# Kernel optimization log

Measured on AMD Instinct MI355X. Metric: run time of the kernel, lower is better.

## Reference

```python
import jax, jax.numpy as jnp
import numpy as np

N, E, T, B = 10000, 80000, 240000, 32
HF, EMB = 256, 64
EDGE_BINS, ANG_BINS = 80, 40
N_CONV = 12  # 4 alignn layers x 2 EGGC + 4 gcn EGGC


def layernorm(x, scale, bias):
    m = x.mean(-1, keepdims=True)
    v = ((x - m) ** 2).mean(-1, keepdims=True)
    return (x - m) / jnp.sqrt(v + 1e-5) * scale + bias


def mlp_layer(x, W, b, ln):
    # Linear -> LayerNorm -> SiLU
    return jax.nn.silu(layernorm(x @ W + b, ln[0], ln[1]))


def rbf(x, vmin, vmax, bins):
    centers = jnp.linspace(vmin, vmax, bins)
    gamma = 0.5 / ((vmax - vmin) / bins) ** 2
    return jnp.exp(-gamma * (x[..., None] - centers) ** 2)


def eggc(W, b, ln_s, ln_b, src, dst, h, e, n_nodes):
    """Edge-gated graph conv. W:[5,F,F] b:[5,F] order: src_gate,dst_gate,edge_gate,src_update,dst_update.
    ln_s/ln_b:[2,F] order: edges, nodes."""
    e_src = h @ W[0] + b[0]
    e_dst = h @ W[1] + b[1]
    sigma = jax.nn.sigmoid(e_src[src] + e_dst[dst] + e @ W[2] + b[2])  # [n_edges, F]
    e_out = layernorm(sigma * e, ln_s[0], ln_b[0])
    Bh = h @ W[4] + b[4]  # dst_update
    sum_sh = jax.ops.segment_sum(Bh[src] * sigma, dst, num_segments=n_nodes)
    sum_s = jax.ops.segment_sum(sigma, dst, num_segments=n_nodes)
    h_out = h @ W[3] + b[3] + sum_sh / (sum_s + 1e-8)  # src_update + gated mean
    return layernorm(h_out, ln_s[1], ln_b[1]), e_out


def setup_inputs() -> dict:
    key = jax.random.key(0)
    ks = jax.random.split(key, 24)
    rn = lambda k, shp: (jax.random.normal(k, shp, dtype=jnp.float32) * 0.05)
    ln_init = lambda f: jnp.stack([jnp.ones((f,), jnp.float32), jnp.zeros((f,), jnp.float32)])
    inp = {
        'atom_features': jax.random.normal(ks[0], (N, 92), dtype=jnp.float32),
        'bondlength': jax.random.uniform(ks[1], (E,), dtype=jnp.float32) * 8.0,
        'angle_h': jax.random.uniform(ks[2], (T,), dtype=jnp.float32) * 2.0 - 1.0,
        'src': jax.random.randint(ks[3], (E,), 0, N, dtype=jnp.int32),
        'dst': jax.random.randint(ks[4], (E,), 0, N, dtype=jnp.int32),
        'lg_src': jax.random.randint(ks[5], (T,), 0, E, dtype=jnp.int32),
        'lg_dst': jax.random.randint(ks[6], (T,), 0, E, dtype=jnp.int32),
        'graph_ids': jnp.sort(jax.random.randint(ks[7], (N,), 0, B)).astype(jnp.int32),
        'atom_W': rn(ks[8], (92, HF)), 'atom_b': jnp.zeros((HF,), jnp.float32), 'atom_ln': ln_init(HF),
        'edge_W1': rn(ks[9], (EDGE_BINS, EMB)), 'edge_b1': jnp.zeros((EMB,), jnp.float32), 'edge_ln1': ln_init(EMB),
        'edge_W2': rn(ks[10], (EMB, HF)), 'edge_b2': jnp.zeros((HF,), jnp.float32), 'edge_ln2': ln_init(HF),
        'ang_W1': rn(ks[11], (ANG_BINS, EMB)), 'ang_b1': jnp.zeros((EMB,), jnp.float32), 'ang_ln1': ln_init(EMB),
        'ang_W2': rn(ks[12], (EMB, HF)), 'ang_b2': jnp.zeros((HF,), jnp.float32), 'ang_ln2': ln_init(HF),
        'conv_W': rn(ks[13], (N_CONV, 5, HF, HF)),
        'conv_b': jnp.zeros((N_CONV, 5, HF), jnp.float32),
        'conv_ln_s': jnp.ones((N_CONV, 2, HF), jnp.float32),
        'conv_ln_b': jnp.zeros((N_CONV, 2, HF), jnp.float32),
    }
    return inp


def reference(atom_features, bondlength, angle_h, src, dst, lg_src, lg_dst, graph_ids,
              atom_W, atom_b, atom_ln, edge_W1, edge_b1, edge_ln1, edge_W2, edge_b2, edge_ln2,
              ang_W1, ang_b1, ang_ln1, ang_W2, ang_b2, ang_ln2,
              conv_W, conv_b, conv_ln_s, conv_ln_b):
    n_nodes = atom_features.shape[0]
    n_edges = bondlength.shape[0]
    # embeddings
    z = mlp_layer(mlp_layer(rbf(angle_h, -1.0, 1.0, ANG_BINS), ang_W1, ang_b1, ang_ln1), ang_W2, ang_b2, ang_ln2)
    x = mlp_layer(atom_features, atom_W, atom_b, atom_ln)
    y = mlp_layer(mlp_layer(rbf(bondlength, 0.0, 8.0, EDGE_BINS), edge_W1, edge_b1, edge_ln1), edge_W2, edge_b2, edge_ln2)
    # 4 ALIGNN layers: edge_update on line graph, then node_update on graph
    for i in range(4):
        j = 2 * i
        y, z = eggc(conv_W[j], conv_b[j], conv_ln_s[j], conv_ln_b[j], lg_src, lg_dst, y, z, n_edges)
        j = 2 * i + 1
        x, y = eggc(conv_W[j], conv_b[j], conv_ln_s[j], conv_ln_b[j], src, dst, x, y, n_nodes)
    # 4 GCN layers
    for i in range(4):
        j = 8 + i
        x, y = eggc(conv_W[j], conv_b[j], conv_ln_s[j], conv_ln_b[j], src, dst, x, y, n_nodes)
    # AvgPooling readout per graph
    sums = jax.ops.segment_sum(x, graph_ids, num_segments=B)
    counts = jax.ops.segment_sum(jnp.ones((n_nodes,), x.dtype), graph_ids, num_segments=B)
    return sums / jnp.maximum(counts, 1.0)[:, None]
```

## Files before the change

kernel.cpp:

```cpp
#include <hip/hip_runtime.h>
#include <hip/hip_bf16.h>

typedef unsigned short u16;
typedef unsigned int u32;
typedef __attribute__((ext_vector_type(8))) short short8;
typedef __attribute__((ext_vector_type(4))) float f32x4;

__device__ __forceinline__ float bf2f(u16 u) { return __uint_as_float(((u32)u) << 16); }
__device__ __forceinline__ u16 f2bf(float f) {
  u32 x = __float_as_uint(f);
  return (u16)((x + 0x7FFFu + ((x >> 16) & 1u)) >> 16);
}
__device__ __forceinline__ void up4(uint2 r, float* o) {
  o[0] = bf2f((u16)(r.x & 0xFFFF)); o[1] = bf2f((u16)(r.x >> 16));
  o[2] = bf2f((u16)(r.y & 0xFFFF)); o[3] = bf2f((u16)(r.y >> 16));
}
__device__ __forceinline__ uint2 pk4(const float* o) {
  uint2 r;
  r.x = (u32)f2bf(o[0]) | ((u32)f2bf(o[1]) << 16);
  r.y = (u32)f2bf(o[2]) | ((u32)f2bf(o[3]) << 16);
  return r;
}
__device__ __forceinline__ void up8(uint4 r, float* o) {
  o[0] = bf2f((u16)(r.x & 0xFFFF)); o[1] = bf2f((u16)(r.x >> 16));
  o[2] = bf2f((u16)(r.y & 0xFFFF)); o[3] = bf2f((u16)(r.y >> 16));
  o[4] = bf2f((u16)(r.z & 0xFFFF)); o[5] = bf2f((u16)(r.z >> 16));
  o[6] = bf2f((u16)(r.w & 0xFFFF)); o[7] = bf2f((u16)(r.w >> 16));
}
__device__ __forceinline__ uint4 pk8(const float* o) {
  uint4 r;
  r.x = (u32)f2bf(o[0]) | ((u32)f2bf(o[1]) << 16);
  r.y = (u32)f2bf(o[2]) | ((u32)f2bf(o[3]) << 16);
  r.z = (u32)f2bf(o[4]) | ((u32)f2bf(o[5]) << 16);
  r.w = (u32)f2bf(o[6]) | ((u32)f2bf(o[7]) << 16);
  return r;
}
__device__ __forceinline__ float wsum64(float v) {
#pragma unroll
  for (int o = 32; o > 0; o >>= 1) v += __shfl_xor(v, o, 64);
  return v;
}
__device__ __forceinline__ float wsum16(float v) {
#pragma unroll
  for (int o = 8; o > 0; o >>= 1) v += __shfl_xor(v, o, 64);
  return v;
}
__device__ __forceinline__ float sigm(float x) { return 1.0f / (1.0f + __expf(-x)); }

__global__ __launch_bounds__(256) void fill_kernel(float* __restrict__ out, int n, float v) {
  int i = blockIdx.x * 256 + threadIdx.x;
  if (i < n) out[i] = v;
}

__global__ __launch_bounds__(256) void wtrans(const float* __restrict__ in,
                                              u16* __restrict__ out, int R, int Ccols) {
  __shared__ float t[64][65];
  const float* ip = in + (size_t)blockIdx.z * R * Ccols;
  u16* op = out + (size_t)blockIdx.z * R * Ccols;
  int kb = blockIdx.x * 64, nb = blockIdx.y * 64;
  int lr = threadIdx.x >> 4, lc = (threadIdx.x & 15) * 4;
#pragma unroll
  for (int p = 0; p < 4; ++p) {
    int k = lr + p * 16;
    float4 v = *(const float4*)(ip + (size_t)(kb + k) * Ccols + nb + lc);
    t[k][lc + 0] = v.x; t[k][lc + 1] = v.y; t[k][lc + 2] = v.z; t[k][lc + 3] = v.w;
  }
  __syncthreads();
#pragma unroll
  for (int p = 0; p < 4; ++p) {
    int n = lr + p * 16;
    uint2 pk;
    pk.x = (u32)f2bf(t[lc + 0][n]) | ((u32)f2bf(t[lc + 1][n]) << 16);
    pk.y = (u32)f2bf(t[lc + 2][n]) | ((u32)f2bf(t[lc + 3][n]) << 16);
    *(uint2*)(op + (size_t)(nb + n) * R + kb + lc) = pk;
  }
}

__global__ __launch_bounds__(256) void csr_hist(const int* __restrict__ dst,
                                                int* __restrict__ hist, int ne) {
  int e = blockIdx.x * 256 + threadIdx.x;
  if (e < ne) atomicAdd(&hist[dst[e]], 1);
}
__global__ __launch_bounds__(1024) void scan1(const int* __restrict__ in,
                                              int* __restrict__ out1, int* __restrict__ bsum, int n) {
  __shared__ int s[1024];
  int i = blockIdx.x * 1024 + threadIdx.x;
  int v = (i < n) ? in[i] : 0;
  s[threadIdx.x] = v; __syncthreads();
  for (int off = 1; off < 1024; off <<= 1) {
    int t = (threadIdx.x >= (u32)off) ? s[threadIdx.x - off] : 0;
    __syncthreads();
    s[threadIdx.x] += t;
    __syncthreads();
  }
  if (i < n) out1[i] = s[threadIdx.x];
  if (threadIdx.x == 1023) bsum[blockIdx.x] = s[1023];
}
__global__ __launch_bounds__(128) void scan2(int* __restrict__ bsum, int nb) {
  __shared__ int s[128];
  int v = (threadIdx.x < (u32)nb) ? bsum[threadIdx.x] : 0;
  s[threadIdx.x] = v; __syncthreads();
  for (int off = 1; off < 128; off <<= 1) {
    int t = (threadIdx.x >= (u32)off) ? s[threadIdx.x - off] : 0;
    __syncthreads();
    s[threadIdx.x] += t;
    __syncthreads();
  }
  if (threadIdx.x < (u32)nb) bsum[threadIdx.x] = threadIdx.x ? s[threadIdx.x - 1] : 0;
}
__global__ __launch_bounds__(256) void scan3(int* __restrict__ offs,
                                             const int* __restrict__ bsum, int n) {
  int i = blockIdx.x * 256 + threadIdx.x;
  if (i == 0) offs[0] = 0;
  if (i < n) offs[1 + i] += bsum[i >> 10];
}
__global__ __launch_bounds__(256) void csr_scatter(const int* __restrict__ dst,
                                                   int* __restrict__ cursor,
                                                   const int* __restrict__ offs,
                                                   int* __restrict__ eid, int ne) {
  int e = blockIdx.x * 256 + threadIdx.x;
  if (e < ne) {
    int d = dst[e];
    int p = offs[d] + atomicAdd(&cursor[d], 1);
    eid[p] = e;
  }
}
__global__ __launch_bounds__(256) void inv_perm(const int* __restrict__ eid,
                                                int* __restrict__ pos, int n) {
  int i = blockIdx.x * 256 + threadIdx.x;
  if (i < n) pos[eid[i]] = i;
}
__global__ __launch_bounds__(256) void remap_k(const int* __restrict__ idx,
                                               const int* __restrict__ map,
                                               int* __restrict__ out, int n) {
  int i = blockIdx.x * 256 + threadIdx.x;
  if (i < n) out[i] = map[idx[i]];
}
__global__ __launch_bounds__(256) void compose_src(const int* __restrict__ eid,
                                                   const int* __restrict__ srcv,
                                                   const int* __restrict__ map,
                                                   int* __restrict__ out, int n) {
  int i = blockIdx.x * 256 + threadIdx.x;
  if (i < n) {
    int s = srcv[eid[i]];
    out[i] = map ? map[s] : s;
  }
}

__global__ __launch_bounds__(256) void embed_s1(
    const float* __restrict__ xin, const float* __restrict__ W1,
    const float* __restrict__ b1, const float* __restrict__ ln1,
    u16* __restrict__ t1, int rows, int bins, float vmin, float vmax,
    const int* __restrict__ perm) {
  int row = (blockIdx.x * 256 + threadIdx.x) >> 6;
  if (row >= rows) return;
  int lane = threadIdx.x & 63;
  float xv = xin[row];
  float rng = vmax - vmin;
  float step = rng / (float)(bins - 1);
  float gamma = 0.5f * ((float)bins / rng) * ((float)bins / rng);
  float rb = 0.f, rb2 = 0.f;
  if (lane < bins) {
    float d = xv - (vmin + lane * step);
    rb = __expf(-gamma * d * d);
  }
  if (bins > 64 && lane < bins - 64) {
    float d = xv - (vmin + (lane + 64) * step);
    rb2 = __expf(-gamma * d * d);
  }
  float u = b1[lane];
  int k1 = bins < 64 ? bins : 64;
  for (int k = 0; k < k1; ++k) {
    float rv = __shfl(rb, k, 64);
    u = fmaf(rv, W1[k * 64 + lane], u);
  }
  for (int k = 64; k < bins; ++k) {
    float rv = __shfl(rb2, k - 64, 64);
    u = fmaf(rv, W1[k * 64 + lane], u);
  }
  float s = wsum64(u), s2 = wsum64(u * u);
  float m = s * (1.f / 64.f), var = s2 * (1.f / 64.f) - m * m;
  float t = (u - m) * rsqrtf(var + 1e-5f) * ln1[lane] + ln1[64 + lane];
  int orow = perm ? perm[row] : row;
  t1[(size_t)orow * 64 + lane] = f2bf(t * sigm(t));
}

__global__ __launch_bounds__(256) void ln_silu(u16* __restrict__ buf,
                                               const float* __restrict__ ln, int rows) {
  int row = (blockIdx.x * 256 + threadIdx.x) >> 6;
  if (row >= rows) return;
  int lane = threadIdx.x & 63;
  int f = lane * 4;
  float v[4];
  up4(*(const uint2*)(buf + (size_t)row * 256 + f), v);
  float s = wsum64(v[0] + v[1] + v[2] + v[3]);
  float s2 = wsum64(v[0] * v[0] + v[1] * v[1] + v[2] * v[2] + v[3] * v[3]);
  float m = s * (1.f / 256.f);
  float rs = rsqrtf(s2 * (1.f / 256.f) - m * m + 1e-5f);
  float o[4];
#pragma unroll
  for (int k = 0; k < 4; ++k) {
    float t = (v[k] - m) * rs * ln[f + k] + ln[256 + f + k];
    o[k] = t * sigm(t);
  }
  *(uint2*)(buf + (size_t)row * 256 + f) = pk4(o);
}

__global__ __launch_bounds__(256) void atom_embed_kernel(
    const float* __restrict__ af, const float* __restrict__ W,
    const float* __restrict__ b, const float* __restrict__ ln,
    u16* __restrict__ out, int rows) {
  int row = blockIdx.x;
  if (row >= rows) return;
  __shared__ float a_s[92];
  __shared__ float red[8];
  int tid = threadIdx.x;
  if (tid < 92) a_s[tid] = af[(size_t)row * 92 + tid];
  __syncthreads();
  float v = b[tid];
#pragma unroll 4
  for (int k = 0; k < 92; ++k) v = fmaf(a_s[k], W[k * 256 + tid], v);
  float s = wsum64(v), s2 = wsum64(v * v);
  int lane = tid & 63, wid = tid >> 6;
  if (lane == 0) { red[wid] = s; red[4 + wid] = s2; }
  __syncthreads();
  s = red[0] + red[1] + red[2] + red[3];
  s2 = red[4] + red[5] + red[6] + red[7];
  float m = s * (1.f / 256.f), var = s2 * (1.f / 256.f) - m * m;
  float t = (v - m) * rsqrtf(var + 1e-5f) * ln[tid] + ln[256 + tid];
  out[(size_t)row * 256 + tid] = f2bf(t * sigm(t));
}

__global__ __launch_bounds__(256) void mfma_gemm(
    const u16* __restrict__ A, const u16* __restrict__ Wt,
    const float* __restrict__ bias, u16* __restrict__ C,
    int M, int K, int ldc, u32 smap) {
  int bm = blockIdx.x * 128;
  if (bm >= M) return;
  int bn = blockIdx.y * 128;
  int slab = (smap >> ((bn >> 8) * 8)) & 0xFF;
  const u16* Wp = Wt + (size_t)slab * 256 * K + (size_t)(bn & 255) * K;
  const float* bp = bias + slab * 256 + (bn & 255);
  int tid = threadIdx.x;
  int w = tid >> 6, lane = tid & 63;
  int q = lane >> 4, r = lane & 15;
  int m0 = (w & 1) * 64;
  int n0 = (w >> 1) * 64;
  const u16* aptr[4];
#pragma unroll
  for (int mi = 0; mi < 4; ++mi) {
    int m = bm + m0 + mi * 16 + r;
    m = m < M - 1 ? m : M - 1;
    aptr[mi] = A + (size_t)m * K + q * 8;
  }
  const u16* wptr[4];
#pragma unroll
  for (int ni = 0; ni < 4; ++ni)
    wptr[ni] = Wp + (size_t)(n0 + ni * 16 + r) * K + q * 8;
  f32x4 acc[4][4] = {};
  for (int kb = 0; kb < K; kb += 32) {
    short8 bfr[4], afr[4];
#pragma unroll
    for (int mi = 0; mi < 4; ++mi) bfr[mi] = *(const short8*)(aptr[mi] + kb);
#pragma unroll
    for (int ni = 0; ni < 4; ++ni) afr[ni] = *(const short8*)(wptr[ni] + kb);
#pragma unroll
    for (int mi = 0; mi < 4; ++mi)
#pragma unroll
      for (int ni = 0; ni < 4; ++ni)
        acc[mi][ni] = __builtin_amdgcn_mfma_f32_16x16x32_bf16(afr[ni], bfr[mi],
                                                              acc[mi][ni], 0, 0, 0);
  }
#pragma unroll
  for (int mi = 0; mi < 4; ++mi) {
    int m = bm + m0 + mi * 16 + r;
    if (m < M) {
#pragma unroll
      for (int ni = 0; ni < 4; ++ni) {
        int n = n0 + ni * 16 + q * 4;
        float4 bv = *(const float4*)(bp + n);
        uint2 o;
        o.x = (u32)f2bf(acc[mi][ni].x + bv.x) | ((u32)f2bf(acc[mi][ni].y + bv.y) << 16);
        o.y = (u32)f2bf(acc[mi][ni].z + bv.z) | ((u32)f2bf(acc[mi][ni].w + bv.w) << 16);
        *(uint2*)(C + (size_t)m * ldc + bn + n) = o;
      }
    }
  }
}

__global__ __launch_bounds__(512) void mega_line(
    u16* __restrict__ h, u16* __restrict__ e, const u16* __restrict__ G0Bh,
    const u16* __restrict__ Wt13, const float* __restrict__ b13,
    const u16* __restrict__ Wt2, const float* __restrict__ b2v,
    const int* __restrict__ src_perm, const int* __restrict__ offs,
    const float* __restrict__ lnS, const float* __restrict__ lnB, int nn) {
  __shared__ u16 g1ah[16][520];
  __shared__ u16 pe[64][264];
  __shared__ int oloc[17];
  int tid = threadIdx.x;
  int w = tid >> 6, lane = tid & 63;
  int q = lane >> 4, r = lane & 15;
  int v0 = blockIdx.x * 16;
  if (tid < 17) { int v = v0 + tid; oloc[tid] = offs[v < nn ? v : nn]; }
  {
    int mrow = v0 + r; if (mrow > nn - 1) mrow = nn - 1;
    const u16* arow = h + (size_t)mrow * 256 + q * 8;
    f32x4 acc[4] = {};
    for (int kb = 0; kb < 256; kb += 32) {
      short8 af = *(const short8*)(arow + kb);
#pragma unroll
      for (int t = 0; t < 4; ++t) {
        int ng = (4 * w + t) * 16 + r;
        const u16* wrow = Wt13 + (size_t)(ng >> 8) * 2 * 65536 +
                          (size_t)(ng & 255) * 256 + q * 8;
        short8 wf = *(const short8*)(wrow + kb);
        acc[t] = __builtin_amdgcn_mfma_f32_16x16x32_bf16(wf, af, acc[t], 0, 0, 0);
      }
    }
#pragma unroll
    for (int t = 0; t < 4; ++t) {
      int nb = (4 * w + t) * 16 + q * 4;
      const float* bp = b13 + (nb >> 8) * 2 * 256 + (nb & 255);
      float o[4] = {acc[t].x + bp[0], acc[t].y + bp[1], acc[t].z + bp[2], acc[t].w + bp[3]};
      *(uint2*)&g1ah[r][nb] = pk4(o);
    }
  }
  __syncthreads();
  int gl = lane & 15;
  int qg = lane >> 4;
  int dd = w * 2 + (qg >> 1);
  int half = qg & 1;
  int vv = v0 + dd;
  int fa = gl * 8;
  int fB = 128 + gl * 8;
  int r0 = oloc[0], r1 = oloc[16];
  int d0 = oloc[dd], d1 = oloc[dd + 1];
  float lwe[16], lbe[16];
#pragma unroll
  for (int k = 0; k < 8; ++k) {
    lwe[k] = lnS[fa + k];     lbe[k] = lnB[fa + k];
    lwe[8 + k] = lnS[fB + k]; lbe[8 + k] = lnB[fB + k];
  }
  uint4 g1p0 = *(const uint4*)&g1ah[dd][fa];
  uint4 g1p1 = *(const uint4*)&g1ah[dd][fB];
  float ssh[16] = {}, ssm[16] = {};

  for (int ec = r0; ec < r1; ec += 64) {
    {
      const u16* w0p = Wt2 + (size_t)((2 * w) * 16 + r) * 256 + q * 8;
      const u16* w1p = Wt2 + (size_t)((2 * w + 1) * 16 + r) * 256 + q * 8;
      f32x4 acc[4][2] = {};
      for (int kb = 0; kb < 256; kb += 32) {
        short8 wf0 = *(const short8*)(w0p + kb);
        short8 wf1 = *(const short8*)(w1p + kb);
#pragma unroll
        for (int mt = 0; mt < 4; ++mt) {
          int erow = ec + mt * 16 + r;
          if (erow > r1 - 1) erow = r1 - 1;
          short8 af = *(const short8*)(e + (size_t)erow * 256 + kb + q * 8);
          acc[mt][0] = __builtin_amdgcn_mfma_f32_16x16x32_bf16(wf0, af, acc[mt][0], 0, 0, 0);
          acc[mt][1] = __builtin_amdgcn_mfma_f32_16x16x32_bf16(wf1, af, acc[mt][1], 0, 0, 0);
        }
      }
#pragma unroll
      for (int mt = 0; mt < 4; ++mt)
#pragma unroll
        for (int nt = 0; nt < 2; ++nt) {
          int nb = (2 * w + nt) * 16 + q * 4;
          float o[4] = {acc[mt][nt].x + b2v[nb], acc[mt][nt].y + b2v[nb + 1],
                        acc[mt][nt].z + b2v[nb + 2], acc[mt][nt].w + b2v[nb + 3]};
          *(uint2*)&pe[mt * 16 + r][nb] = pk4(o);
        }
    }
    __syncthreads();
    {
      int ce = ec + 64 < r1 ? ec + 64 : r1;
      int i0 = d0 > ec ? d0 : ec;
      int i1 = d1 < ce ? d1 : ce;
      int is = i0 + half;
      if (is < i1) {
        int sv = src_perm[is];
        uint4 pg0a = *(const uint4*)(G0Bh + (size_t)sv * 512 + fa);
        uint4 pg0b = *(const uint4*)(G0Bh + (size_t)sv * 512 + fB);
        uint4 pbha = *(const uint4*)(G0Bh + (size_t)sv * 512 + 256 + fa);
        uint4 pbhb = *(const uint4*)(G0Bh + (size_t)sv * 512 + 256 + fB);
        for (int i = is; i < i1; i += 2) {
          uint4 cg0a = pg0a, cg0b = pg0b, cbha = pbha, cbhb = pbhb;
          if (i + 2 < i1) {
            int sv2 = src_perm[i + 2];
            pg0a = *(const uint4*)(G0Bh + (size_t)sv2 * 512 + fa);
            pg0b = *(const uint4*)(G0Bh + (size_t)sv2 * 512 + fB);
            pbha = *(const uint4*)(G0Bh + (size_t)sv2 * 512 + 256 + fa);
            pbhb = *(const uint4*)(G0Bh + (size_t)sv2 * 512 + 256 + fB);
          }
          float g0[16], bh[16], pv[16], ev[16], g1v[16];
          up8(cg0a, g0); up8(cg0b, g0 + 8);
          up8(cbha, bh); up8(cbhb, bh + 8);
          up8(*(const uint4*)&pe[i - ec][fa], pv);
          up8(*(const uint4*)&pe[i - ec][fB], pv + 8);
          up8(*(const uint4*)(e + (size_t)i * 256 + fa), ev);
          up8(*(const uint4*)(e + (size_t)i * 256 + fB), ev + 8);
          up8(g1p0, g1v); up8(g1p1, g1v + 8);
          float t[16];
          float ssum = 0.f, s2sum = 0.f;
#pragma unroll
          for (int k = 0; k < 16; ++k) {
            float sg = sigm(g0[k] + g1v[k] + pv[k]);
            t[k] = sg * ev[k];
            ssh[k] = fmaf(bh[k], sg, ssh[k]);
            ssm[k] += sg;
            ssum += t[k]; s2sum += t[k] * t[k];
          }
          float s1 = wsum16(ssum), s2 = wsum16(s2sum);
          float mn = s1 * (1.f / 256.f);
          float rs = rsqrtf(s2 * (1.f / 256.f) - mn * mn + 1e-5f);
          float o[16];
#pragma unroll
          for (int k = 0; k < 16; ++k) o[k] = (t[k] - mn) * rs * lwe[k] + lbe[k];
          *(uint4*)(e + (size_t)i * 256 + fa) = pk8(o);
          *(uint4*)(e + (size_t)i * 256 + fB) = pk8(o + 8);
        }
      }
    }
    __syncthreads();
  }
#pragma unroll
  for (int k = 0; k < 16; ++k) {
    ssh[k] += __shfl_xor(ssh[k], 16, 64);
    ssm[k] += __shfl_xor(ssm[k], 16, 64);
  }
  if (half == 0 && vv < nn) {
    float ah[16], tt[16];
    up8(*(const uint4*)&g1ah[dd][256 + fa], ah);
    up8(*(const uint4*)&g1ah[dd][256 + fB], ah + 8);
    float ssum = 0.f, s2sum = 0.f;
#pragma unroll
    for (int k = 0; k < 16; ++k) {
      tt[k] = ah[k] + ssh[k] / (ssm[k] + 1e-8f);
      ssum += tt[k]; s2sum += tt[k] * tt[k];
    }
    float s1 = wsum16(ssum), s2 = wsum16(s2sum);
    float mn = s1 * (1.f / 256.f);
    float rs = rsqrtf(s2 * (1.f / 256.f) - mn * mn + 1e-5f);
    float o[16];
#pragma unroll
    for (int k = 0; k < 8; ++k) {
      o[k] = (tt[k] - mn) * rs * lnS[256 + fa + k] + lnB[256 + fa + k];
      o[8 + k] = (tt[8 + k] - mn) * rs * lnS[256 + fB + k] + lnB[256 + fB + k];
    }
    *(uint4*)(h + (size_t)vv * 256 + fa) = pk8(o);
    *(uint4*)(h + (size_t)vv * 256 + fB) = pk8(o + 8);
  }
}

__global__ __launch_bounds__(256) void mega_atom(
    u16* __restrict__ h, u16* __restrict__ e, const u16* __restrict__ GAll,
    const u16* __restrict__ Pe,
    const int* __restrict__ src_perm, const int* __restrict__ offs,
    const float* __restrict__ lnS, const float* __restrict__ lnB, int nn) {
  __shared__ int oloc[9];
  int tid = threadIdx.x;
  int w = tid >> 6, lane = tid & 63;
  int v0 = blockIdx.x * 8;
  if (tid < 9) { int v = v0 + tid; oloc[tid] = offs[v < nn ? v : nn]; }
  __syncthreads();
  int gl = lane & 15;
  int qg = lane >> 4;
  int dd = w * 2 + (qg >> 1);
  int half = qg & 1;
  int vv = v0 + dd;
  int fa = gl * 8;
  int fB = 128 + gl * 8;
  int d0 = oloc[dd], d1 = oloc[dd + 1];
  float lwe[16], lbe[16];
#pragma unroll
  for (int k = 0; k < 8; ++k) {
    lwe[k] = lnS[fa + k];     lbe[k] = lnB[fa + k];
    lwe[8 + k] = lnS[fB + k]; lbe[8 + k] = lnB[fB + k];
  }
  int vc = vv < nn ? vv : nn - 1;
  uint4 g1p0 = *(const uint4*)(GAll + (size_t)vc * 1024 + 256 + fa);
  uint4 g1p1 = *(const uint4*)(GAll + (size_t)vc * 1024 + 256 + fB);
  float ssh[16] = {}, ssm[16] = {};

  int is = d0 + half;
  if (is < d1) {
    int sv = src_perm[is];
    uint4 pg0a = *(const uint4*)(GAll + (size_t)sv * 1024 + fa);
    uint4 pg0b = *(const uint4*)(GAll + (size_t)sv * 1024 + fB);
    uint4 pbha = *(const uint4*)(GAll + (size_t)sv * 1024 + 768 + fa);
    uint4 pbhb = *(const uint4*)(GAll + (size_t)sv * 1024 + 768 + fB);
    for (int i = is; i < d1; i += 2) {
      uint4 cg0a = pg0a, cg0b = pg0b, cbha = pbha, cbhb = pbhb;
      if (i + 2 < d1) {
        int sv2 = src_perm[i + 2];
        pg0a = *(const uint4*)(GAll + (size_t)sv2 * 1024 + fa);
        pg0b = *(const uint4*)(GAll + (size_t)sv2 * 1024 + fB);
        pbha = *(const uint4*)(GAll + (size_t)sv2 * 1024 + 768 + fa);
        pbhb = *(const uint4*)(GAll + (size_t)sv2 * 1024 + 768 + fB);
      }
      float g0[16], bh[16], pv[16], ev[16], g1v[16];
      up8(cg0a, g0); up8(cg0b, g0 + 8);
      up8(cbha, bh); up8(cbhb, bh + 8);
      up8(*(const uint4*)(Pe + (size_t)i * 256 + fa), pv);
      up8(*(const uint4*)(Pe + (size_t)i * 256 + fB), pv + 8);
      up8(*(const uint4*)(e + (size_t)i * 256 + fa), ev);
      up8(*(const uint4*)(e + (size_t)i * 256 + fB), ev + 8);
      up8(g1p0, g1v); up8(g1p1, g1v + 8);
      float t[16];
      float ssum = 0.f, s2sum = 0.f;
#pragma unroll
      for (int k = 0; k < 16; ++k) {
        float sg = sigm(g0[k] + g1v[k] + pv[k]);
        t[k] = sg * ev[k];
        ssh[k] = fmaf(bh[k], sg, ssh[k]);
        ssm[k] += sg;
        ssum += t[k]; s2sum += t[k] * t[k];
      }
      float s1 = wsum16(ssum), s2 = wsum16(s2sum);
      float mn = s1 * (1.f / 256.f);
      float rs = rsqrtf(s2 * (1.f / 256.f) - mn * mn + 1e-5f);
      float o[16];
#pragma unroll
      for (int k = 0; k < 16; ++k) o[k] = (t[k] - mn) * rs * lwe[k] + lbe[k];
      *(uint4*)(e + (size_t)i * 256 + fa) = pk8(o);
      *(uint4*)(e + (size_t)i * 256 + fB) = pk8(o + 8);
    }
  }
#pragma unroll
  for (int k = 0; k < 16; ++k) {
    ssh[k] += __shfl_xor(ssh[k], 16, 64);
    ssm[k] += __shfl_xor(ssm[k], 16, 64);
  }
  if (half == 0 && vv < nn) {
    float ah[16], tt[16];
    up8(*(const uint4*)(GAll + (size_t)vv * 1024 + 512 + fa), ah);
    up8(*(const uint4*)(GAll + (size_t)vv * 1024 + 512 + fB), ah + 8);
    float ssum = 0.f, s2sum = 0.f;
#pragma unroll
    for (int k = 0; k < 16; ++k) {
      tt[k] = ah[k] + ssh[k] / (ssm[k] + 1e-8f);
      ssum += tt[k]; s2sum += tt[k] * tt[k];
    }
    float s1 = wsum16(ssum), s2 = wsum16(s2sum);
    float mn = s1 * (1.f / 256.f);
    float rs = rsqrtf(s2 * (1.f / 256.f) - mn * mn + 1e-5f);
    float o[16];
#pragma unroll
    for (int k = 0; k < 8; ++k) {
      o[k] = (tt[k] - mn) * rs * lnS[256 + fa + k] + lnB[256 + fa + k];
      o[8 + k] = (tt[8 + k] - mn) * rs * lnS[256 + fB + k] + lnB[256 + fB + k];
    }
    *(uint4*)(h + (size_t)vv * 256 + fa) = pk8(o);
    *(uint4*)(h + (size_t)vv * 256 + fB) = pk8(o + 8);
  }
}

__global__ __launch_bounds__(256) void pool_acc(
    const u16* __restrict__ x, const int* __restrict__ gid,
    float* __restrict__ out, float* __restrict__ cnt, int n) {
  int v = (blockIdx.x * 256 + threadIdx.x) >> 6;
  if (v >= n) return;
  int lane = threadIdx.x & 63;
  int f = lane * 4;
  int g = gid[v];
  float xv[4];
  up4(*(const uint2*)(x + (size_t)v * 256 + f), xv);
  float* p = out + (size_t)g * 256 + f;
  unsafeAtomicAdd(p + 0, xv[0]);
  unsafeAtomicAdd(p + 1, xv[1]);
  unsafeAtomicAdd(p + 2, xv[2]);
  unsafeAtomicAdd(p + 3, xv[3]);
  if (lane == 0) unsafeAtomicAdd(cnt + g, 1.0f);
}
__global__ __launch_bounds__(256) void pool_div(float* __restrict__ out,
                                                const float* __restrict__ cnt, int n) {
  int i = blockIdx.x * blockDim.x + threadIdx.x;
  if (i < n) out[i] /= fmaxf(cnt[i >> 8], 1.0f);
}

extern "C" void kernel_launch(void* const* d_in, const int* in_sizes, int n_in,
                              void* d_out, int out_size, void* d_ws, size_t ws_size,
                              hipStream_t stream) {
  const float* atom_features = (const float*)d_in[0];
  const float* bondlength    = (const float*)d_in[1];
  const float* angle_h       = (const float*)d_in[2];
  const int*   src           = (const int*)d_in[3];
  const int*   dst           = (const int*)d_in[4];
  const int*   lg_src        = (const int*)d_in[5];
  const int*   lg_dst        = (const int*)d_in[6];
  const int*   gid           = (const int*)d_in[7];
  const float* atom_W  = (const float*)d_in[8];
  const float* atom_b  = (const float*)d_in[9];
  const float* atom_ln = (const float*)d_in[10];
  const float* edge_W1 = (const float*)d_in[11];
  const float* edge_b1 = (const float*)d_in[12];
  const float* edge_ln1= (const float*)d_in[13];
  const float* edge_W2 = (const float*)d_in[14];
  const float* edge_b2 = (const float*)d_in[15];
  const float* edge_ln2= (const float*)d_in[16];
  const float* ang_W1  = (const float*)d_in[17];
  const float* ang_b1  = (const float*)d_in[18];
  const float* ang_ln1 = (const float*)d_in[19];
  const float* ang_W2  = (const float*)d_in[20];
  const float* ang_b2  = (const float*)d_in[21];
  const float* ang_ln2 = (const float*)d_in[22];
  const float* conv_W  = (const float*)d_in[23];
  const float* conv_b  = (const float*)d_in[24];
  const float* conv_lns= (const float*)d_in[25];
  const float* conv_lnb= (const float*)d_in[26];

  int N = in_sizes[0] / 92;
  int E = in_sizes[1];
  int T = in_sizes[2];

  char* ws = (char*)d_ws;
  size_t o = 0;
  auto alloc = [&](size_t bytes) { size_t r = o; o = (o + bytes + 255) & ~(size_t)255; return r; };
  u16* z     = (u16*)(ws + alloc((size_t)T * 512));
  u16* y     = (u16*)(ws + alloc((size_t)E * 512));
  u16* x     = (u16*)(ws + alloc((size_t)N * 512));
  int* offsL = (int*)(ws + alloc((size_t)(E + 1) * 4));
  int* offsA = (int*)(ws + alloc((size_t)(N + 1) * 4));
  int* spL   = (int*)(ws + alloc((size_t)T * 4));
  int* spA   = (int*)(ws + alloc((size_t)E * 4));
  int* pA    = (int*)(ws + alloc((size_t)E * 4));
  int* pL    = (int*)(ws + alloc((size_t)T * 4));
  int* eidL  = (int*)(ws + alloc((size_t)T * 4));
  int* eidA  = (int*)(ws + alloc((size_t)E * 4));
  int* ldSt  = (int*)(ws + alloc((size_t)T * 4));
  int* tmp   = (int*)(ws + alloc((size_t)(E > N ? E : N) * 4));
  int* bsum  = (int*)(ws + alloc(1024));
  float* cnt = (float*)(ws + alloc(1024));
  u16* WtAll = (u16*)(ws + alloc((size_t)12 * 5 * 65536 * 2));
  u16* WtAng = (u16*)(ws + alloc((size_t)16384 * 2));
  u16* WtEdg = (u16*)(ws + alloc((size_t)16384 * 2));
  size_t scratch_base = o;
  size_t need = scratch_base + (size_t)E * 1024;
  {
    size_t atom_need = scratch_base + (size_t)N * 2048 + (size_t)E * 512;
    if (atom_need > need) need = atom_need;
    size_t embed_need = scratch_base + ((size_t)T + E) * 128;
    if (embed_need > need) need = embed_need;
  }
  if (ws_size < need) {
    fill_kernel<<<(out_size + 255) / 256, 256, 0, stream>>>(
        (float*)d_out, out_size, (float)(ws_size >> 20));
    return;
  }

  wtrans<<<dim3(4, 4, 60), 256, 0, stream>>>(conv_W, WtAll, 256, 256);
  wtrans<<<dim3(1, 4, 1), 256, 0, stream>>>(ang_W2, WtAng, 64, 256);
  wtrans<<<dim3(1, 4, 1), 256, 0, stream>>>(edge_W2, WtEdg, 64, 256);

  auto build_csr = [&](const int* dvec, int ne_, int nn_, int* offs_, int* eid_) {
    hipMemsetAsync(tmp, 0, (size_t)nn_ * 4, stream);
    csr_hist<<<(ne_ + 255) / 256, 256, 0, stream>>>(dvec, tmp, ne_);
    int nb = (nn_ + 1023) / 1024;
    scan1<<<nb, 1024, 0, stream>>>(tmp, offs_ + 1, bsum, nn_);
    scan2<<<1, 128, 0, stream>>>(bsum, nb);
    scan3<<<(nn_ + 255) / 256, 256, 0, stream>>>(offs_, bsum, nn_);
    hipMemsetAsync(tmp, 0, (size_t)nn_ * 4, stream);
    csr_scatter<<<(ne_ + 255) / 256, 256, 0, stream>>>(dvec, tmp, offs_, eid_, ne_);
  };
  build_csr(dst, E, N, offsA, eidA);
  inv_perm<<<(E + 255) / 256, 256, 0, stream>>>(eidA, pA, E);
  compose_src<<<(E + 255) / 256, 256, 0, stream>>>(eidA, src, nullptr, spA, E);
  remap_k<<<(T + 255) / 256, 256, 0, stream>>>(lg_dst, pA, ldSt, T);
  build_csr(ldSt, T, E, offsL, eidL);
  inv_perm<<<(T + 255) / 256, 256, 0, stream>>>(eidL, pL, T);
  compose_src<<<(T + 255) / 256, 256, 0, stream>>>(eidL, lg_src, pA, spL, T);

  u16* t1T = (u16*)(ws + scratch_base);
  u16* t1E = t1T + (size_t)T * 64;
  embed_s1<<<(T + 3) / 4, 256, 0, stream>>>(angle_h, ang_W1, ang_b1, ang_ln1,
                                            t1T, T, 40, -1.f, 1.f, pL);
  embed_s1<<<(E + 3) / 4, 256, 0, stream>>>(bondlength, edge_W1, edge_b1, edge_ln1,
                                            t1E, E, 80, 0.f, 8.f, pA);
  mfma_gemm<<<dim3((T + 127) / 128, 2), 256, 0, stream>>>(
      t1T, WtAng, ang_b2, z, T, 64, 256, 0u);
  mfma_gemm<<<dim3((E + 127) / 128, 2), 256, 0, stream>>>(
      t1E, WtEdg, edge_b2, y, E, 64, 256, 0u);
  ln_silu<<<(T + 3) / 4, 256, 0, stream>>>(z, ang_ln2, T);
  ln_silu<<<(E + 3) / 4, 256, 0, stream>>>(y, edge_ln2, E);
  atom_embed_kernel<<<N, 256, 0, stream>>>(atom_features, atom_W, atom_b, atom_ln, x, N);

  for (int l = 0; l < 12; ++l) {
    const u16* WtL  = WtAll + (size_t)l * 5 * 65536;
    const float* bl = conv_b + (size_t)l * 5 * 256;
    const float* lnS = conv_lns + (size_t)l * 512;
    const float* lnB = conv_lnb + (size_t)l * 512;
    bool line = (l < 8) && ((l & 1) == 0);
    if (line) {
      u16* G0Bh = (u16*)(ws + scratch_base);
      mfma_gemm<<<dim3((E + 127) / 128, 4), 256, 0, stream>>>(
          y, WtL, bl, G0Bh, E, 256, 512, 0u | (4u << 8));
      mega_line<<<(E + 15) / 16, 512, 0, stream>>>(
          y, z, G0Bh, WtL + 65536, bl + 256, WtL + 2 * 65536, bl + 2 * 256,
          spL, offsL, lnS, lnB, E);
    } else {
      u16* GAll = (u16*)(ws + scratch_base);
      u16* PeA  = GAll + (size_t)N * 1024;
      mfma_gemm<<<dim3((N + 127) / 128, 8), 256, 0, stream>>>(
          x, WtL, bl, GAll, N, 256, 1024, 0u | (1u << 8) | (3u << 16) | (4u << 24));
      mfma_gemm<<<dim3((E + 127) / 128, 2), 256, 0, stream>>>(
          y, WtL + 2 * 65536, bl + 2 * 256, PeA, E, 256, 256, 0u);
      mega_atom<<<(N + 7) / 8, 256, 0, stream>>>(
          x, y, GAll, PeA, spA, offsA, lnS, lnB, N);
    }
  }

  hipMemsetAsync(d_out, 0, (size_t)out_size * sizeof(float), stream);
  hipMemsetAsync(cnt, 0, 256 * sizeof(float), stream);
  pool_acc<<<(N + 3) / 4, 256, 0, stream>>>(x, gid, (float*)d_out, cnt, N);
  pool_div<<<(out_size + 255) / 256, 256, 0, stream>>>((float*)d_out, cnt, out_size);
}
```

Baseline: 4.677 ms.

## Halve line-graph edge chunk and stage edge outputs through shared memory

The fused line-graph kernel now processes edges in chunks of 32 instead of 64. Each wave computes one 16-row by 64-column tile of the edge-gate GEMM instead of all 64 rows by 32 columns. Updated edge features are written to a second shared buffer and then copied to global memory in coalesced full-row stores, replacing scattered 16-byte writes. This is meant to cut register pressure and improve the write pattern, at the cost of more chunk iterations and barriers and more redundant weight loads per row.

```diff
diff --git a/kernel.cpp b/kernel.cpp
--- a/kernel.cpp
+++ b/kernel.cpp
@@ -295,7 +295,8 @@
     const int* __restrict__ src_perm, const int* __restrict__ offs,
     const float* __restrict__ lnS, const float* __restrict__ lnB, int nn) {
   __shared__ u16 g1ah[16][520];
-  __shared__ u16 pe[64][264];
+  __shared__ u16 pe[32][264];
+  __shared__ u16 pe2[32][264];
   __shared__ int oloc[17];
   int tid = threadIdx.x;
   int w = tid >> 6, lane = tid & 63;
@@ -345,36 +346,32 @@
   uint4 g1p1 = *(const uint4*)&g1ah[dd][fB];
   float ssh[16] = {}, ssm[16] = {};
 
-  for (int ec = r0; ec < r1; ec += 64) {
+  for (int ec = r0; ec < r1; ec += 32) {
     {
-      const u16* w0p = Wt2 + (size_t)((2 * w) * 16 + r) * 256 + q * 8;
-      const u16* w1p = Wt2 + (size_t)((2 * w + 1) * 16 + r) * 256 + q * 8;
-      f32x4 acc[4][2] = {};
+      int mt = w & 1, ng = w >> 1;
+      int er = ec + mt * 16 + r; if (er > r1 - 1) er = r1 - 1;
+      const u16* ap = e + (size_t)er * 256 + q * 8;
+      f32x4 acc[4] = {};
       for (int kb = 0; kb < 256; kb += 32) {
-        short8 wf0 = *(const short8*)(w0p + kb);
-        short8 wf1 = *(const short8*)(w1p + kb);
-#pragma unroll
-        for (int mt = 0; mt < 4; ++mt) {
-          int erow = ec + mt * 16 + r;
-          if (erow > r1 - 1) erow = r1 - 1;
-          short8 af = *(const short8*)(e + (size_t)erow * 256 + kb + q * 8);
-          acc[mt][0] = __builtin_amdgcn_mfma_f32_16x16x32_bf16(wf0, af, acc[mt][0], 0, 0, 0);
-          acc[mt][1] = __builtin_amdgcn_mfma_f32_16x16x32_bf16(wf1, af, acc[mt][1], 0, 0, 0);
+        short8 af = *(const short8*)(ap + kb);
+#pragma unroll
+        for (int t = 0; t < 4; ++t) {
+          const u16* wp = Wt2 + (size_t)((ng * 4 + t) * 16 + r) * 256 + q * 8;
+          short8 wf = *(const short8*)(wp + kb);
+          acc[t] = __builtin_amdgcn_mfma_f32_16x16x32_bf16(wf, af, acc[t], 0, 0, 0);
         }
       }
 #pragma unroll
-      for (int mt = 0; mt < 4; ++mt)
-#pragma unroll
-        for (int nt = 0; nt < 2; ++nt) {
-          int nb = (2 * w + nt) * 16 + q * 4;
-          float o[4] = {acc[mt][nt].x + b2v[nb], acc[mt][nt].y + b2v[nb + 1],
-                        acc[mt][nt].z + b2v[nb + 2], acc[mt][nt].w + b2v[nb + 3]};
-          *(uint2*)&pe[mt * 16 + r][nb] = pk4(o);
-        }
+      for (int t = 0; t < 4; ++t) {
+        int nb = (ng * 4 + t) * 16 + q * 4;
+        float o[4] = {acc[t].x + b2v[nb], acc[t].y + b2v[nb + 1],
+                      acc[t].z + b2v[nb + 2], acc[t].w + b2v[nb + 3]};
+        *(uint2*)&pe[mt * 16 + r][nb] = pk4(o);
+      }
     }
     __syncthreads();
     {
-      int ce = ec + 64 < r1 ? ec + 64 : r1;
+      int ce = ec + 32 < r1 ? ec + 32 : r1;
       int i0 = d0 > ec ? d0 : ec;
       int i1 = d1 < ce ? d1 : ce;
       int is = i0 + half;
@@ -417,12 +414,23 @@
           float o[16];
 #pragma unroll
           for (int k = 0; k < 16; ++k) o[k] = (t[k] - mn) * rs * lwe[k] + lbe[k];
-          *(uint4*)(e + (size_t)i * 256 + fa) = pk8(o);
-          *(uint4*)(e + (size_t)i * 256 + fB) = pk8(o + 8);
+          *(uint4*)&pe2[i - ec][fa] = pk8(o);
+          *(uint4*)&pe2[i - ec][fB] = pk8(o + 8);
         }
       }
     }
     __syncthreads();
+    {
+      int ce = ec + 32 < r1 ? ec + 32 : r1;
+#pragma unroll
+      for (int rr = 0; rr < 4; ++rr) {
+        int t = w * 4 + rr;
+        int i = ec + t;
+        if (i < ce) {
+          *(uint2*)(e + (size_t)i * 256 + lane * 4) = *(const uint2*)&pe2[t][lane * 4];
+        }
+      }
+    }
   }
 #pragma unroll
   for (int k = 0; k < 16; ++k) {
```

After: 6.432 ms. 1.38x slower.
